# Performance work log

Measured on AMD Instinct MI355X. Metric: run time of the kernel, lower is better.

## Reference

```python
import jax, jax.numpy as jnp
import numpy as np

B, S, D, H, HD = 4, 1024, 512, 8, 64  # batch, seq_len, hidden_dim, n_heads, head_dim
N_DIL = min(5, H)


def _head_masks(seq_len: int, n_heads: int) -> jnp.ndarray:
    """Log-sparse banded+dilated masks, shape [n_heads, S, S] (bool)."""
    i = jnp.arange(seq_len)
    diff = jnp.abs(i[:, None] - i[None, :])  # [S, S]
    masks = jnp.stack([
        (diff <= 2 ** h) | (diff % (2 ** (h + 1)) == 0)
        for h in range(N_DIL)
    ])  # [N_DIL, S, S]
    idx = [min(h, N_DIL - 1) for h in range(n_heads)]
    return masks[jnp.asarray(idx)]  # [H, S, S]


def setup_inputs() -> dict:
    key = jax.random.key(0)
    ks = jax.random.split(key, 9)
    sc = 0.02
    return {
        "x": jax.random.normal(ks[0], (B, S, D), jnp.float32),
        "Wq": jax.random.normal(ks[1], (H, D, HD), jnp.float32) * sc,
        "bq": jax.random.normal(ks[2], (H, HD), jnp.float32) * sc,
        "Wk": jax.random.normal(ks[3], (H, D, HD), jnp.float32) * sc,
        "bk": jax.random.normal(ks[4], (H, HD), jnp.float32) * sc,
        "Wv": jax.random.normal(ks[5], (H, D, HD), jnp.float32) * sc,
        "bv": jax.random.normal(ks[6], (H, HD), jnp.float32) * sc,
        "Wo": jax.random.normal(ks[7], (D, D), jnp.float32) * sc,
        "bo": jax.random.normal(ks[8], (D,), jnp.float32) * sc,
    }


def reference(x, Wq, bq, Wk, bk, Wv, bv, Wo, bo):
    b, s, d = x.shape
    h, _, hd = Wq.shape
    # Per-head projections (batched over heads).
    q = jnp.einsum("bsd,hde->bhse", x, Wq) + bq[None, :, None, :]
    k = jnp.einsum("bsd,hde->bhse", x, Wk) + bk[None, :, None, :]
    v = jnp.einsum("bsd,hde->bhse", x, Wv) + bv[None, :, None, :]
    scores = jnp.einsum("bhse,bhte->bhst", q, k) / (hd ** 0.5)
    mask = _head_masks(s, h)  # [H, S, S] bool; diagonal always allowed
    scores = jnp.where(mask[None], scores, -jnp.inf)
    probs = jax.nn.softmax(scores, axis=-1)  # dropout is identity in eval
    out = jnp.einsum("bhst,bhte->bhse", probs, v)
    concat = out.transpose(0, 2, 1, 3).reshape(b, s, d)  # heads concatenated
    return concat @ Wo + bo
```

## Files before the change

### kernel.cpp

```cpp
#include <hip/hip_runtime.h>

typedef unsigned short u16;
typedef unsigned int u32;
typedef __attribute__((ext_vector_type(8))) __bf16 bf16x8;
typedef __attribute__((ext_vector_type(4))) float f32x4;
typedef __attribute__((ext_vector_type(16))) float f32x16;
typedef __attribute__((ext_vector_type(4))) u32 u32x4;

#if __has_builtin(__builtin_amdgcn_exp2f)
#define EXP2F(x) __builtin_amdgcn_exp2f(x)
#else
#define EXP2F(x) exp2f(x)
#endif

#define SC_Q 0.18033688011112042f

static __device__ __forceinline__ u16 f2bf(float f) {
  unsigned u = __builtin_bit_cast(unsigned, f);
  u += 0x7fffu + ((u >> 16) & 1u);
  return (u16)(u >> 16);
}
static __device__ __forceinline__ float bf2f(u16 v) {
  return __builtin_bit_cast(float, (u32)v << 16);
}

static __device__ __forceinline__ f32x4 mfma16(bf16x8 a, bf16x8 b, f32x4 c) {
  return __builtin_amdgcn_mfma_f32_16x16x32_bf16(a, b, c, 0, 0, 0);
}
static __device__ __forceinline__ f32x16 mfma32(bf16x8 a, bf16x8 b, f32x16 c) {
  return __builtin_amdgcn_mfma_f32_32x32x16_bf16(a, b, c, 0, 0, 0);
}

static __device__ __forceinline__ u32 cvtpk(float lo, float hi_) {
  u32 r;
  asm("v_cvt_pk_bf16_f32 %0, %1, %2" : "=v"(r) : "v"(lo), "v"(hi_));
  return r;
}

static __device__ __forceinline__ void barrier_raw() {
  asm volatile("" ::: "memory");
  __builtin_amdgcn_s_barrier();
  asm volatile("" ::: "memory");
}

static __device__ __forceinline__ void gload_lds16(const u16* g, u16* l) {
  __builtin_amdgcn_global_load_lds((const __attribute__((address_space(1))) u32*)g,
                                   (__attribute__((address_space(3))) u32*)l, 16, 0, 0);
}

__global__ void pack_w_kernel(const float* __restrict__ Wq, const float* __restrict__ Wk,
                              const float* __restrict__ Wv, const float* __restrict__ Wo,
                              const float* __restrict__ bq, const float* __restrict__ bk,
                              const float* __restrict__ bv, u16* __restrict__ BTqkv,
                              u16* __restrict__ BTo, float* __restrict__ bqkv) {
  int idx = blockIdx.x * 256 + threadIdx.x;
  if (idx < 1536 * 512) {
    int n = idx >> 9, d = idx & 511;
    int t = n >> 9, rem = n & 511;
    int h = rem >> 6, e = rem & 63;
    const float* W = (t == 0) ? Wq : ((t == 1) ? Wk : Wv);
    float sc = (t == 0) ? SC_Q : 1.0f;
    BTqkv[idx] = f2bf(W[((size_t)h * 512 + d) * 64 + e] * sc);
  } else if (idx < 1536 * 512 + 512 * 512) {
    int j = idx - 1536 * 512;
    int n = j >> 9, d = j & 511;
    BTo[j] = f2bf(Wo[(size_t)d * 512 + n]);
  } else if (idx < 1536 * 512 + 512 * 512 + 1536) {
    int j = idx - (1536 * 512 + 512 * 512);
    int t = j >> 9, rem = j & 511;
    float v = (t == 0 ? bq : (t == 1 ? bk : bv))[rem];
    bqkv[j] = v * (t == 0 ? SC_Q : 1.0f);
  }
}

__global__ __launch_bounds__(256) void gemm_qkv_kernel(const float* __restrict__ X,
                                                       const u16* __restrict__ BT,
                                                       const float* __restrict__ bias,
                                                       u16* __restrict__ QK,
                                                       u16* __restrict__ Vtl) {
  __shared__ __align__(16) u16 Al[2][128 * 64];
  __shared__ __align__(16) u16 Bl[2][64 * 64];
  const int K = 512;
  const int tid = threadIdx.x;
  const int w = tid >> 6, lane = tid & 63, g = lane >> 4, i = lane & 15;
  const int m0 = blockIdx.x * 128, n0 = blockIdx.y * 64;
  const int wr = (w >> 1) * 64, wc = (w & 1) * 32;

  f32x4 acc[4][2];
#pragma unroll
  for (int a = 0; a < 4; ++a)
#pragma unroll
    for (int b = 0; b < 2; ++b) acc[a][b] = f32x4{0.f, 0.f, 0.f, 0.f};

  const float* xg[4];
#pragma unroll
  for (int it = 0; it < 4; ++it) {
    const int slot = it * 256 + tid;
    xg[it] = X + (size_t)(m0 + (slot >> 3)) * K + (slot & 7) * 8;
  }
  const u16* bgp[2];
#pragma unroll
  for (int it = 0; it < 2; ++it) {
    const int slot = it * 256 + tid;
    bgp[it] = BT + (size_t)(n0 + (slot >> 3)) * K + (slot & 7) * 8;
  }

  float4 a0[4], a1[4];
#pragma unroll
  for (int it = 0; it < 4; ++it) {
    a0[it] = *reinterpret_cast<const float4*>(xg[it]);
    a1[it] = *reinterpret_cast<const float4*>(xg[it] + 4);
  }
#pragma unroll
  for (int it = 0; it < 2; ++it) gload_lds16(bgp[it], &Bl[0][(it * 256 + tid) * 8]);
  asm volatile("s_waitcnt vmcnt(2)" ::: "memory");
#pragma unroll
  for (int it = 0; it < 4; ++it) {
    u32x4 pk = {cvtpk(a0[it].x, a0[it].y), cvtpk(a0[it].z, a0[it].w),
                cvtpk(a1[it].x, a1[it].y), cvtpk(a1[it].z, a1[it].w)};
    *reinterpret_cast<u32x4*>(&Al[0][(it * 256 + tid) * 8]) = pk;
  }
  asm volatile("s_waitcnt lgkmcnt(0)" ::: "memory");

  int cur = 0;
  for (int t = 0; t < 8; ++t) {
    const int k0 = t * 64;
    if (t < 7) {
#pragma unroll
      for (int it = 0; it < 4; ++it) {
        a0[it] = *reinterpret_cast<const float4*>(xg[it] + k0 + 64);
        a1[it] = *reinterpret_cast<const float4*>(xg[it] + k0 + 68);
      }
#pragma unroll
      for (int it = 0; it < 2; ++it)
        gload_lds16(bgp[it] + k0 + 64, &Bl[cur ^ 1][(it * 256 + tid) * 8]);
      asm volatile("s_waitcnt vmcnt(10)" ::: "memory");
    } else {
      asm volatile("s_waitcnt vmcnt(0)" ::: "memory");
    }
    barrier_raw();
#pragma unroll
    for (int ks = 0; ks < 2; ++ks) {
      bf16x8 af[4], bf[2];
#pragma unroll
      for (int mf = 0; mf < 4; ++mf)
        af[mf] = *reinterpret_cast<const bf16x8*>(
            &Al[cur][(wr + mf * 16 + i) * 64 + ks * 32 + 8 * g]);
#pragma unroll
      for (int nf = 0; nf < 2; ++nf)
        bf[nf] = *reinterpret_cast<const bf16x8*>(
            &Bl[cur][(wc + nf * 16 + i) * 64 + ks * 32 + 8 * g]);
#pragma unroll
      for (int mf = 0; mf < 4; ++mf)
#pragma unroll
        for (int nf = 0; nf < 2; ++nf) acc[mf][nf] = mfma16(af[mf], bf[nf], acc[mf][nf]);
    }
    if (t < 7) {
      asm volatile("s_waitcnt vmcnt(2)" ::: "memory");
#pragma unroll
      for (int it = 0; it < 4; ++it) {
        u32x4 pk = {cvtpk(a0[it].x, a0[it].y), cvtpk(a0[it].z, a0[it].w),
                    cvtpk(a1[it].x, a1[it].y), cvtpk(a1[it].z, a1[it].w)};
        *reinterpret_cast<u32x4*>(&Al[cur ^ 1][(it * 256 + tid) * 8]) = pk;
      }
      asm volatile("s_waitcnt lgkmcnt(0)" ::: "memory");
    }
    barrier_raw();
    cur ^= 1;
  }

  if (n0 < 1024) {
#pragma unroll
    for (int nf = 0; nf < 2; ++nf) {
      const int col = n0 + wc + nf * 16 + i;
      const float bb = bias[col];
#pragma unroll
      for (int mf = 0; mf < 4; ++mf) {
#pragma unroll
        for (int r = 0; r < 4; ++r) {
          const int row = m0 + wr + mf * 16 + 4 * g + r;
          QK[(size_t)row * 1024 + col] = f2bf(acc[mf][nf][r] + bb);
        }
      }
    }
  } else {
    const int b = m0 >> 10;
    const int s0b = (m0 & 1023) + wr;
#pragma unroll
    for (int nf = 0; nf < 2; ++nf) {
      const int col = n0 + wc + nf * 16 + i;
      const float bb = bias[col];
      const int vcol = col - 1024;
      const size_t rowb = (size_t)(b * 512 + vcol) * 1024;
#pragma unroll
      for (int mf = 0; mf < 4; ++mf) {
        u16 pk[4];
#pragma unroll
        for (int r = 0; r < 4; ++r) pk[r] = f2bf(acc[mf][nf][r] + bb);
        const int ss = s0b + mf * 16 + 4 * g;
        *reinterpret_cast<uint2*>(&Vtl[rowb + ss]) = *reinterpret_cast<const uint2*>(pk);
      }
    }
  }
}

__global__ __launch_bounds__(256) void attn3_kernel(const u16* __restrict__ QK,
                                                    const u16* __restrict__ Vt,
                                                    u16* __restrict__ Opart16,
                                                    float* __restrict__ mlpart) {
  __shared__ __align__(16) u16 Kl[2][4096];
  __shared__ __align__(16) u16 Vl[2][4096];

  const int tid = threadIdx.x;
  const int w = tid >> 6, lane = tid & 63;
  const int col = lane & 31, hi = lane >> 5;
  const int h = blockIdx.x;
  const int zz = blockIdx.z;
  const int b = zz >> 1, s = zz & 1;
  const int bh = b * 8 + h;
  const int q0w = blockIdx.y * 128 + w * 32;
  const int kvlo = s * 512;
  const int hm = (h < 4) ? h : 4;
  const int band = 1 << hm;
  const int modm = (2 << hm) - 1;
  const int qrow = q0w + col;

  bf16x8 qf[4];
  const size_t qoff = (size_t)(b * 1024 + qrow) * 1024 + h * 64 + 8 * hi;
#pragma unroll
  for (int et = 0; et < 4; ++et)
    qf[et] = *reinterpret_cast<const bf16x8*>(QK + qoff + 16 * et);

  float bias[16];
#pragma unroll
  for (int r = 0; r < 16; ++r) {
    int c = (r & 3) + 8 * (r >> 2) + 4 * hi;
    bias[r] = (((qrow - c) & modm) == 0) ? 0.f : -1e30f;
  }

  f32x16 accO0 = {}, accO1 = {};
  float m_run = -1e30f, l_run = 0.f;

  const int slot0 = tid, slot1 = tid + 256;
  const int kj0 = slot0 >> 3, keb0 = (slot0 & 7) ^ (kj0 & 7);
  const int kj1 = slot1 >> 3, keb1 = (slot1 & 7) ^ (kj1 & 7);
  const u16* kg0 = QK + (size_t)(b * 1024 + kj0) * 1024 + 512 + h * 64 + keb0 * 8;
  const u16* kg1 = QK + (size_t)(b * 1024 + kj1) * 1024 + 512 + h * 64 + keb1 * 8;
  const u16* vg0 = Vt + (size_t)(bh * 64 + kj0) * 1024 + keb0 * 8;
  const u16* vg1 = Vt + (size_t)(bh * 64 + kj1) * 1024 + keb1 * 8;

#define STAGE3(bi, kv0)                                                 \
  do {                                                                  \
    gload_lds16(kg0 + (size_t)(kv0) * 1024, &Kl[bi][slot0 * 8]);        \
    gload_lds16(kg1 + (size_t)(kv0) * 1024, &Kl[bi][slot1 * 8]);        \
    gload_lds16(vg0 + (kv0), &Vl[bi][slot0 * 8]);                       \
    gload_lds16(vg1 + (kv0), &Vl[bi][slot1 * 8]);                       \
  } while (0)

  STAGE3(0, kvlo);
  int buf = 0;

  for (int t = 0; t < 8; ++t) {
    const int kv0 = kvlo + t * 64;
    if (t < 7) {
      STAGE3(buf ^ 1, kv0 + 64);
      asm volatile("s_waitcnt vmcnt(4)" ::: "memory");
    } else {
      asm volatile("s_waitcnt vmcnt(0)" ::: "memory");
    }
    barrier_raw();

    const u16* Kb = Kl[buf];
    const u16* Vb = Vl[buf];

    f32x16 s0 = {}, s1 = {};
    __builtin_amdgcn_s_setprio(1);
#pragma unroll
    for (int et = 0; et < 4; ++et) {
      const int sw = ((2 * et + hi) ^ (col & 7)) << 3;
      bf16x8 kf0 = *reinterpret_cast<const bf16x8*>(&Kb[col * 64 + sw]);
      bf16x8 kf1 = *reinterpret_cast<const bf16x8*>(&Kb[(col + 32) * 64 + sw]);
      s0 = mfma32(kf0, qf[et], s0);
      s1 = mfma32(kf1, qf[et], s1);
    }
    __builtin_amdgcn_s_setprio(0);

    float p[32];
    const int dq = qrow - kv0;
    const bool near = (q0w <= kv0 + 63 + band) && (kv0 <= q0w + 31 + band);
    if (near) {
#pragma unroll
      for (int r = 0; r < 16; ++r) {
        const int c = (r & 3) + 8 * (r >> 2) + 4 * hi;
        int d0 = dq - c, d1 = d0 - 32;
        d0 = d0 < 0 ? -d0 : d0;
        d1 = d1 < 0 ? -d1 : d1;
        p[r] = (d0 <= band) ? s0[r] : s0[r] + bias[r];
        p[r + 16] = (d1 <= band) ? s1[r] : s1[r] + bias[r];
      }
    } else {
#pragma unroll
      for (int r = 0; r < 16; ++r) {
        p[r] = s0[r] + bias[r];
        p[r + 16] = s1[r] + bias[r];
      }
    }

    float tr[16];
#pragma unroll
    for (int j = 0; j < 16; ++j) tr[j] = fmaxf(p[j], p[j + 16]);
#pragma unroll
    for (int st = 8; st >= 1; st >>= 1)
#pragma unroll
      for (int j = 0; j < st; ++j) tr[j] = fmaxf(tr[j], tr[j + st]);
    float mu = fmaxf(tr[0], __shfl_xor(tr[0], 32));

    if (__any(mu > m_run + 8.f)) {
      float mn = fmaxf(m_run, mu);
      float corr = EXP2F(m_run - mn);
      m_run = mn;
      l_run *= corr;
#pragma unroll
      for (int j = 0; j < 16; ++j) {
        accO0[j] *= corr;
        accO1[j] *= corr;
      }
    }

#pragma unroll
    for (int j = 0; j < 32; ++j) p[j] = EXP2F(p[j] - m_run);
    float ts[16];
#pragma unroll
    for (int j = 0; j < 16; ++j) ts[j] = p[j] + p[j + 16];
#pragma unroll
    for (int st = 8; st >= 1; st >>= 1)
#pragma unroll
      for (int j = 0; j < st; ++j) ts[j] += ts[j + st];
    l_run += ts[0] + __shfl_xor(ts[0], 32);

#pragma unroll
    for (int kt = 0; kt < 4; ++kt) {
      const float* pp = (kt < 2) ? p : p + 16;
      const int R = (kt & 1) * 8;
      u32 A0 = cvtpk(pp[R + 0], pp[R + 1]);
      u32 A1 = cvtpk(pp[R + 2], pp[R + 3]);
      u32 B0 = cvtpk(pp[R + 4], pp[R + 5]);
      u32 B1 = cvtpk(pp[R + 6], pp[R + 7]);
      u32 t0 = __shfl_xor(hi ? A0 : B0, 32);
      u32 t1 = __shfl_xor(hi ? A1 : B1, 32);
      u32 w0 = hi ? t0 : A0;
      u32 w1 = hi ? t1 : A1;
      u32 w2 = hi ? B0 : t0;
      u32 w3 = hi ? B1 : t1;
      u32x4 pu = {w0, w1, w2, w3};
      bf16x8 paf = __builtin_bit_cast(bf16x8, pu);
      const int jb = 2 * kt + hi;
      __builtin_amdgcn_s_setprio(1);
      {
        const int erow = col;
        bf16x8 vf = *reinterpret_cast<const bf16x8*>(&Vb[erow * 64 + ((jb ^ (erow & 7)) << 3)]);
        accO0 = mfma32(paf, vf, accO0);
      }
      {
        const int erow = 32 + col;
        bf16x8 vf = *reinterpret_cast<const bf16x8*>(&Vb[erow * 64 + ((jb ^ (erow & 7)) << 3)]);
        accO1 = mfma32(paf, vf, accO1);
      }
      __builtin_amdgcn_s_setprio(0);
    }

    barrier_raw();
    buf ^= 1;
  }
#undef STAGE3

  const size_t obase = (size_t)(s * 32 + bh) * 1024 + q0w;
  if (lane < 32) {
    float2 ml2 = {m_run, l_run};
    *reinterpret_cast<float2*>(&mlpart[(obase + col) * 2]) = ml2;
  }
#pragma unroll
  for (int r = 0; r < 16; ++r) {
    const int c = (r & 3) + 8 * (r >> 2) + 4 * hi;
    u16* orow = Opart16 + (obase + c) * 64;
    orow[col] = f2bf(accO0[r]);
    orow[32 + col] = f2bf(accO1[r]);
  }
}

__global__ __launch_bounds__(256) void gemm_out_kernel(const u16* __restrict__ Opart16,
                                                       const float* __restrict__ mlpart,
                                                       const u16* __restrict__ BT,
                                                       const float* __restrict__ bias,
                                                       float* __restrict__ Cf) {
  __shared__ __align__(16) u16 Al[2][64 * 64];
  __shared__ __align__(16) u16 Bl[2][64 * 64];
  const int K = 512;
  const int tid = threadIdx.x;
  const int w = tid >> 6, lane = tid & 63, g = lane >> 4, i = lane & 15;
  const int m0 = blockIdx.x * 64, n0 = blockIdx.y * 64;
  const int wr = (w >> 1) * 32, wc = (w & 1) * 32;

  f32x4 acc[2][2];
#pragma unroll
  for (int a = 0; a < 2; ++a)
#pragma unroll
    for (int b = 0; b < 2; ++b) acc[a][b] = f32x4{0.f, 0.f, 0.f, 0.f};

  size_t R0[2];
  int cb8[2];
#pragma unroll
  for (int it = 0; it < 2; ++it) {
    const int slot = it * 256 + tid;
    const int r_in = slot >> 3;
    cb8[it] = (slot & 7) * 8;
    const int grow = m0 + r_in;
    const int b2 = grow >> 10, qr = grow & 1023;
    R0[it] = (size_t)(b2 * 8) * 1024 + qr;
  }
  const u16* bgp[2];
#pragma unroll
  for (int it = 0; it < 2; ++it) {
    const int slot = it * 256 + tid;
    bgp[it] = BT + (size_t)(n0 + (slot >> 3)) * K + (slot & 7) * 8;
  }

  uint4 aO[2][2];
  float2 aml[2][2];

#define LOAD_A(t)                                                                     \
  do {                                                                                \
    _Pragma("unroll") for (int it = 0; it < 2; ++it) {                                \
      _Pragma("unroll") for (int s2 = 0; s2 < 2; ++s2) {                              \
        const size_t rb = R0[it] + (size_t)(s2 * 32 + (t)) * 1024;                    \
        aO[it][s2] = *reinterpret_cast<const uint4*>(&Opart16[rb * 64 + cb8[it]]);    \
        aml[it][s2] = *reinterpret_cast<const float2*>(&mlpart[rb * 2]);              \
      }                                                                               \
    }                                                                                 \
  } while (0)

#define COMBINE_WRITE(bi)                                                             \
  do {                                                                                \
    _Pragma("unroll") for (int it = 0; it < 2; ++it) {                                \
      const float mA = aml[it][0].x, lA = aml[it][0].y;                               \
      const float mB = aml[it][1].x, lB = aml[it][1].y;                               \
      const float M2 = fmaxf(mA, mB);                                                 \
      const float wA = EXP2F(mA - M2), wB = EXP2F(mB - M2);                           \
      const float inv = 1.0f / (lA * wA + lB * wB);                                   \
      const float sA = wA * inv, sB = wB * inv;                                       \
      const u32* oa = reinterpret_cast<const u32*>(&aO[it][0]);                       \
      const u32* ob = reinterpret_cast<const u32*>(&aO[it][1]);                       \
      float c[8];                                                                     \
      _Pragma("unroll") for (int q = 0; q < 4; ++q) {                                 \
        c[2 * q] = bf2f((u16)(oa[q] & 0xffff)) * sA + bf2f((u16)(ob[q] & 0xffff)) * sB; \
        c[2 * q + 1] = bf2f((u16)(oa[q] >> 16)) * sA + bf2f((u16)(ob[q] >> 16)) * sB; \
      }                                                                               \
      u32x4 pk = {cvtpk(c[0], c[1]), cvtpk(c[2], c[3]), cvtpk(c[4], c[5]),            \
                  cvtpk(c[6], c[7])};                                                 \
      *reinterpret_cast<u32x4*>(&Al[bi][(it * 256 + tid) * 8]) = pk;                  \
    }                                                                                 \
  } while (0)

  LOAD_A(0);
#pragma unroll
  for (int it = 0; it < 2; ++it) gload_lds16(bgp[it], &Bl[0][(it * 256 + tid) * 8]);
  asm volatile("s_waitcnt vmcnt(2)" ::: "memory");
  COMBINE_WRITE(0);
  asm volatile("s_waitcnt lgkmcnt(0)" ::: "memory");

  int cur = 0;
  for (int t = 0; t < 8; ++t) {
    if (t < 7) {
      LOAD_A(t + 1);
#pragma unroll
      for (int it = 0; it < 2; ++it)
        gload_lds16(bgp[it] + t * 64 + 64, &Bl[cur ^ 1][(it * 256 + tid) * 8]);
      asm volatile("s_waitcnt vmcnt(10)" ::: "memory");
    } else {
      asm volatile("s_waitcnt vmcnt(0)" ::: "memory");
    }
    barrier_raw();
#pragma unroll
    for (int ks = 0; ks < 2; ++ks) {
      bf16x8 af[2], bf[2];
#pragma unroll
      for (int mf = 0; mf < 2; ++mf)
        af[mf] = *reinterpret_cast<const bf16x8*>(
            &Al[cur][(wr + mf * 16 + i) * 64 + ks * 32 + 8 * g]);
#pragma unroll
      for (int nf = 0; nf < 2; ++nf)
        bf[nf] = *reinterpret_cast<const bf16x8*>(
            &Bl[cur][(wc + nf * 16 + i) * 64 + ks * 32 + 8 * g]);
#pragma unroll
      for (int mf = 0; mf < 2; ++mf)
#pragma unroll
        for (int nf = 0; nf < 2; ++nf) acc[mf][nf] = mfma16(af[mf], bf[nf], acc[mf][nf]);
    }
    if (t < 7) {
      asm volatile("s_waitcnt vmcnt(2)" ::: "memory");
      COMBINE_WRITE(cur ^ 1);
      asm volatile("s_waitcnt lgkmcnt(0)" ::: "memory");
    }
    barrier_raw();
    cur ^= 1;
  }
#undef LOAD_A
#undef COMBINE_WRITE

#pragma unroll
  for (int nf = 0; nf < 2; ++nf) {
    const int col = n0 + wc + nf * 16 + i;
    const float bb = bias[col];
#pragma unroll
    for (int mf = 0; mf < 2; ++mf) {
#pragma unroll
      for (int r = 0; r < 4; ++r) {
        const int row = m0 + wr + mf * 16 + 4 * g + r;
        Cf[(size_t)row * 512 + col] = acc[mf][nf][r] + bb;
      }
    }
  }
}

extern "C" void kernel_launch(void* const* d_in, const int* in_sizes, int n_in,
                              void* d_out, int out_size, void* d_ws, size_t ws_size,
                              hipStream_t stream) {
  const float* x = (const float*)d_in[0];
  const float* Wq = (const float*)d_in[1];
  const float* bq = (const float*)d_in[2];
  const float* Wk = (const float*)d_in[3];
  const float* bk = (const float*)d_in[4];
  const float* Wv = (const float*)d_in[5];
  const float* bv = (const float*)d_in[6];
  const float* Wo = (const float*)d_in[7];
  const float* bo = (const float*)d_in[8];
  float* out = (float*)d_out;

  char* ws = (char*)d_ws;
  u16* BTqkv = (u16*)(ws + (4u << 20));
  u16* BTo = (u16*)(ws + (6u << 20));
  float* bqkv = (float*)(ws + (7u << 20));
  u16* QK = (u16*)(ws + (8u << 20));
  u16* Vtl = (u16*)(ws + (21u << 20));
  u16* Opart16 = (u16*)(ws + (32u << 20));
  float* mlpart = (float*)(ws + (56u << 20));

  const int NW = 1536 * 512 + 512 * 512 + 1536;
  pack_w_kernel<<<(NW + 255) / 256, 256, 0, stream>>>(Wq, Wk, Wv, Wo, bq, bk, bv, BTqkv,
                                                      BTo, bqkv);

  gemm_qkv_kernel<<<dim3(32, 24), 256, 0, stream>>>(x, BTqkv, bqkv, QK, Vtl);

  attn3_kernel<<<dim3(8, 8, 8), 256, 0, stream>>>(QK, Vtl, Opart16, mlpart);

  gemm_out_kernel<<<dim3(64, 8), 256, 0, stream>>>(Opart16, mlpart, BTo, bo, out);
}
```

Before: 63.47 us.

## Split heads 4-7 attention into dilated and band kernels with permuted V layout

Heads 4-7 share the dilation-32 plus band-16 mask, so their attention is split into two specialized kernels. attnD computes the stride-32 dilated part over residue classes using a permuted V copy written by the QKV GEMM. attnB computes the band part |d| between 1 and 16 over a 64-key window. The generic attn3 kernel now covers only heads 0-3. This avoids scanning many masked-out tiles, at the cost of an extra scattered V write and two more launches, and it relies on the partial-softmax merge in gemm_out to combine the split segments.

After: 80.00 us. 1.26x slower.

```diff
diff --git a/kernel.cpp b/kernel.cpp
--- a/kernel.cpp
+++ b/kernel.cpp
@@ -77,7 +77,8 @@
                                                        const u16* __restrict__ BT,
                                                        const float* __restrict__ bias,
                                                        u16* __restrict__ QK,
-                                                       u16* __restrict__ Vtl) {
+                                                       u16* __restrict__ Vtl,
+                                                       u16* __restrict__ Vtp) {
   __shared__ __align__(16) u16 Al[2][128 * 64];
   __shared__ __align__(16) u16 Bl[2][64 * 64];
   const int K = 512;
@@ -191,6 +192,10 @@
       const int col = n0 + wc + nf * 16 + i;
       const float bb = bias[col];
       const int vcol = col - 1024;
+      const int hh = vcol >> 6;
+      const int hmm = (hh < 4) ? hh : 4;
+      const int Mlog = hmm + 1;
+      const int NcH = 1024 >> Mlog;
       const size_t rowb = (size_t)(b * 512 + vcol) * 1024;
 #pragma unroll
       for (int mf = 0; mf < 4; ++mf) {
@@ -199,6 +204,12 @@
         for (int r = 0; r < 4; ++r) pk[r] = f2bf(acc[mf][nf][r] + bb);
         const int ss = s0b + mf * 16 + 4 * g;
         *reinterpret_cast<uint2*>(&Vtl[rowb + ss]) = *reinterpret_cast<const uint2*>(pk);
+#pragma unroll
+        for (int r = 0; r < 4; ++r) {
+          const int seq = ss + r;
+          const int pidx = (seq & ((1 << Mlog) - 1)) * NcH + (seq >> Mlog);
+          Vtp[rowb + pidx] = pk[r];
+        }
       }
     }
   }
@@ -388,6 +399,263 @@
   }
 }
 
+__global__ __launch_bounds__(256) void attnD_kernel(const u16* __restrict__ QK,
+                                                    const u16* __restrict__ Vtp,
+                                                    u16* __restrict__ Opart16,
+                                                    float* __restrict__ mlpart) {
+  __shared__ __align__(16) u16 Kl[4][32 * 72];
+  __shared__ __align__(16) u16 Vl[4][64 * 40];
+
+  const int tid = threadIdx.x;
+  const int w = tid >> 6, lane = tid & 63;
+  const int col = lane & 31, hi = lane >> 5;
+  const int h = 4 + blockIdx.x;
+  const int qblk = blockIdx.y, b = blockIdx.z;
+  const int M = 32;
+  const int cls = qblk * 4 + w;
+  const int bh = b * 8 + h;
+
+  for (int sl = lane; sl < 256; sl += 64) {
+    const int kj = sl >> 3, eb = sl & 7;
+    const int physk = cls + kj * M;
+    bf16x8 kreg = *reinterpret_cast<const bf16x8*>(
+        QK + (size_t)(b * 1024 + physk) * 1024 + 512 + h * 64 + eb * 8);
+    *reinterpret_cast<bf16x8*>(&Kl[w][kj * 72 + eb * 8]) = kreg;
+  }
+  for (int sl = lane; sl < 256; sl += 64) {
+    const int e = sl >> 2, tb = sl & 3;
+    bf16x8 vreg = *reinterpret_cast<const bf16x8*>(
+        Vtp + (size_t)(b * 512 + h * 64 + e) * 1024 + cls * 32 + tb * 8);
+    *reinterpret_cast<bf16x8*>(&Vl[w][e * 40 + tb * 8]) = vreg;
+  }
+
+  const int physq = cls + col * M;
+  bf16x8 qf[4];
+  const size_t qoff = (size_t)(b * 1024 + physq) * 1024 + h * 64 + 8 * hi;
+#pragma unroll
+  for (int et = 0; et < 4; ++et)
+    qf[et] = *reinterpret_cast<const bf16x8*>(QK + qoff + 16 * et);
+
+  __syncthreads();
+
+  f32x16 s0 = {};
+  __builtin_amdgcn_s_setprio(1);
+#pragma unroll
+  for (int et = 0; et < 4; ++et) {
+    const int sw8 = (2 * et + hi) * 8;
+    bf16x8 kf0 = *reinterpret_cast<const bf16x8*>(&Kl[w][col * 72 + sw8]);
+    s0 = mfma32(kf0, qf[et], s0);
+  }
+  __builtin_amdgcn_s_setprio(0);
+
+  float p[32];
+#pragma unroll
+  for (int r = 0; r < 16; ++r) {
+    p[r] = s0[r];
+    p[r + 16] = -1e30f;
+  }
+  float tr[16];
+#pragma unroll
+  for (int j = 0; j < 16; ++j) tr[j] = fmaxf(p[j], p[j + 16]);
+#pragma unroll
+  for (int st = 8; st >= 1; st >>= 1)
+#pragma unroll
+    for (int j = 0; j < st; ++j) tr[j] = fmaxf(tr[j], tr[j + st]);
+  const float mu = fmaxf(tr[0], __shfl_xor(tr[0], 32));
+
+#pragma unroll
+  for (int j = 0; j < 32; ++j) p[j] = EXP2F(p[j] - mu);
+  float ts[16];
+#pragma unroll
+  for (int j = 0; j < 16; ++j) ts[j] = p[j] + p[j + 16];
+#pragma unroll
+  for (int st = 8; st >= 1; st >>= 1)
+#pragma unroll
+    for (int j = 0; j < st; ++j) ts[j] += ts[j + st];
+  const float l = ts[0] + __shfl_xor(ts[0], 32);
+
+  f32x16 accO0 = {}, accO1 = {};
+  const u16* Vb = &Vl[w][0];
+#pragma unroll
+  for (int kt = 0; kt < 2; ++kt) {
+    const float* pp = p;
+    const int R = (kt & 1) * 8;
+    u32 A0 = cvtpk(pp[R + 0], pp[R + 1]);
+    u32 A1 = cvtpk(pp[R + 2], pp[R + 3]);
+    u32 B0 = cvtpk(pp[R + 4], pp[R + 5]);
+    u32 B1 = cvtpk(pp[R + 6], pp[R + 7]);
+    u32 t0 = __shfl_xor(hi ? A0 : B0, 32);
+    u32 t1 = __shfl_xor(hi ? A1 : B1, 32);
+    u32 w0 = hi ? t0 : A0;
+    u32 w1 = hi ? t1 : A1;
+    u32 w2 = hi ? B0 : t0;
+    u32 w3 = hi ? B1 : t1;
+    u32x4 pu = {w0, w1, w2, w3};
+    bf16x8 paf = __builtin_bit_cast(bf16x8, pu);
+    const int jb = 2 * kt + hi;
+    __builtin_amdgcn_s_setprio(1);
+    {
+      const int erow = col;
+      bf16x8 vf = *reinterpret_cast<const bf16x8*>(&Vb[erow * 40 + (jb << 3)]);
+      accO0 = mfma32(paf, vf, accO0);
+    }
+    {
+      const int erow = 32 + col;
+      bf16x8 vf = *reinterpret_cast<const bf16x8*>(&Vb[erow * 40 + (jb << 3)]);
+      accO1 = mfma32(paf, vf, accO1);
+    }
+    __builtin_amdgcn_s_setprio(0);
+  }
+
+  const size_t pb = (size_t)(1 * 32 + bh) * 1024;
+  if (lane < 32) {
+    float2 ml2 = {mu, l};
+    *reinterpret_cast<float2*>(&mlpart[(pb + physq) * 2]) = ml2;
+  }
+#pragma unroll
+  for (int r = 0; r < 16; ++r) {
+    const int cf = (r & 3) + 8 * (r >> 2) + 4 * hi;
+    const int physr = cls + cf * M;
+    u16* orow = Opart16 + (pb + physr) * 64;
+    orow[col] = f2bf(accO0[r]);
+    orow[32 + col] = f2bf(accO1[r]);
+  }
+}
+
+__global__ __launch_bounds__(256) void attnB_kernel(const u16* __restrict__ QK,
+                                                    const u16* __restrict__ Vtl,
+                                                    u16* __restrict__ Opart16,
+                                                    float* __restrict__ mlpart) {
+  __shared__ __align__(16) u16 Kl[4][64 * 72];
+  __shared__ __align__(16) u16 Vl[4][64 * 72];
+
+  const int tid = threadIdx.x;
+  const int w = tid >> 6, lane = tid & 63;
+  const int col = lane & 31, hi = lane >> 5;
+  const int h = 4 + blockIdx.x;
+  const int qt = blockIdx.y, b = blockIdx.z;
+  const int bh = b * 8 + h;
+  const int band = 16;
+  const int q0w = qt * 128 + w * 32;
+  const int qrow = q0w + col;
+  int kw = q0w - 16;
+  kw = kw < 0 ? 0 : (kw > 960 ? 960 : kw);
+
+  for (int sl = tid; sl < 2048; sl += 256) {
+    const int wv = sl >> 9, s9 = sl & 511;
+    int kwv = qt * 128 + wv * 32 - 16;
+    kwv = kwv < 0 ? 0 : (kwv > 960 ? 960 : kwv);
+    const int kj = s9 >> 3, eb = s9 & 7;
+    bf16x8 kreg = *reinterpret_cast<const bf16x8*>(
+        QK + (size_t)(b * 1024 + kwv + kj) * 1024 + 512 + h * 64 + eb * 8);
+    *reinterpret_cast<bf16x8*>(&Kl[wv][kj * 72 + eb * 8]) = kreg;
+    bf16x8 vreg = *reinterpret_cast<const bf16x8*>(
+        Vtl + (size_t)(b * 512 + h * 64 + kj) * 1024 + kwv + eb * 8);
+    *reinterpret_cast<bf16x8*>(&Vl[wv][kj * 72 + eb * 8]) = vreg;
+  }
+
+  bf16x8 qf[4];
+  const size_t qoff = (size_t)(b * 1024 + qrow) * 1024 + h * 64 + 8 * hi;
+#pragma unroll
+  for (int et = 0; et < 4; ++et)
+    qf[et] = *reinterpret_cast<const bf16x8*>(QK + qoff + 16 * et);
+
+  f32x16 accO0 = {}, accO1 = {};
+
+  __syncthreads();
+
+  const u16* Kb = &Kl[w][0];
+  const u16* Vb = &Vl[w][0];
+
+  f32x16 s0 = {}, s1 = {};
+  __builtin_amdgcn_s_setprio(1);
+#pragma unroll
+  for (int et = 0; et < 4; ++et) {
+    const int sw8 = (2 * et + hi) * 8;
+    bf16x8 kf0 = *reinterpret_cast<const bf16x8*>(&Kb[col * 72 + sw8]);
+    bf16x8 kf1 = *reinterpret_cast<const bf16x8*>(&Kb[(col + 32) * 72 + sw8]);
+    s0 = mfma32(kf0, qf[et], s0);
+    s1 = mfma32(kf1, qf[et], s1);
+  }
+  __builtin_amdgcn_s_setprio(0);
+
+  float p[32];
+  const int dq = qrow - kw;
+#pragma unroll
+  for (int r = 0; r < 16; ++r) {
+    const int cf = (r & 3) + 8 * (r >> 2) + 4 * hi;
+    const int d0 = dq - cf, d1 = d0 - 32;
+    const int a0 = d0 < 0 ? -d0 : d0;
+    const int a1 = d1 < 0 ? -d1 : d1;
+    p[r] = (a0 >= 1 && a0 <= band) ? s0[r] : -1e30f;
+    p[r + 16] = (a1 >= 1 && a1 <= band) ? s1[r] : -1e30f;
+  }
+
+  float tr[16];
+#pragma unroll
+  for (int j = 0; j < 16; ++j) tr[j] = fmaxf(p[j], p[j + 16]);
+#pragma unroll
+  for (int st = 8; st >= 1; st >>= 1)
+#pragma unroll
+    for (int j = 0; j < st; ++j) tr[j] = fmaxf(tr[j], tr[j + st]);
+  const float mu = fmaxf(tr[0], __shfl_xor(tr[0], 32));
+
+#pragma unroll
+  for (int j = 0; j < 32; ++j) p[j] = EXP2F(p[j] - mu);
+  float ts[16];
+#pragma unroll
+  for (int j = 0; j < 16; ++j) ts[j] = p[j] + p[j + 16];
+#pragma unroll
+  for (int st = 8; st >= 1; st >>= 1)
+#pragma unroll
+    for (int j = 0; j < st; ++j) ts[j] += ts[j + st];
+  const float l = ts[0] + __shfl_xor(ts[0], 32);
+
+#pragma unroll
+  for (int kt = 0; kt < 4; ++kt) {
+    const float* pp = (kt < 2) ? p : p + 16;
+    const int R = (kt & 1) * 8;
+    u32 A0 = cvtpk(pp[R + 0], pp[R + 1]);
+    u32 A1 = cvtpk(pp[R + 2], pp[R + 3]);
+    u32 B0 = cvtpk(pp[R + 4], pp[R + 5]);
+    u32 B1 = cvtpk(pp[R + 6], pp[R + 7]);
+    u32 t0 = __shfl_xor(hi ? A0 : B0, 32);
+    u32 t1 = __shfl_xor(hi ? A1 : B1, 32);
+    u32 w0 = hi ? t0 : A0;
+    u32 w1 = hi ? t1 : A1;
+    u32 w2 = hi ? B0 : t0;
+    u32 w3 = hi ? B1 : t1;
+    u32x4 pu = {w0, w1, w2, w3};
+    bf16x8 paf = __builtin_bit_cast(bf16x8, pu);
+    const int jb = 2 * kt + hi;
+    __builtin_amdgcn_s_setprio(1);
+    {
+      const int erow = col;
+      bf16x8 vf = *reinterpret_cast<const bf16x8*>(&Vb[erow * 72 + (jb << 3)]);
+      accO0 = mfma32(paf, vf, accO0);
+    }
+    {
+      const int erow = 32 + col;
+      bf16x8 vf = *reinterpret_cast<const bf16x8*>(&Vb[erow * 72 + (jb << 3)]);
+      accO1 = mfma32(paf, vf, accO1);
+    }
+    __builtin_amdgcn_s_setprio(0);
+  }
+
+  const size_t pb = (size_t)bh * 1024;
+  if (lane < 32) {
+    float2 ml2 = {mu, l};
+    *reinterpret_cast<float2*>(&mlpart[(pb + qrow) * 2]) = ml2;
+  }
+#pragma unroll
+  for (int r = 0; r < 16; ++r) {
+    const int cf = (r & 3) + 8 * (r >> 2) + 4 * hi;
+    u16* orow = Opart16 + (pb + q0w + cf) * 64;
+    orow[col] = f2bf(accO0[r]);
+    orow[32 + col] = f2bf(accO1[r]);
+  }
+}
+
 __global__ __launch_bounds__(256) void gemm_out_kernel(const u16* __restrict__ Opart16,
                                                        const float* __restrict__ mlpart,
                                                        const u16* __restrict__ BT,
@@ -542,6 +810,7 @@
   float* bqkv = (float*)(ws + (7u << 20));
   u16* QK = (u16*)(ws + (8u << 20));
   u16* Vtl = (u16*)(ws + (21u << 20));
+  u16* Vtp = (u16*)(ws + (25u << 20));
   u16* Opart16 = (u16*)(ws + (32u << 20));
   float* mlpart = (float*)(ws + (56u << 20));
 
@@ -549,9 +818,11 @@
   pack_w_kernel<<<(NW + 255) / 256, 256, 0, stream>>>(Wq, Wk, Wv, Wo, bq, bk, bv, BTqkv,
                                                       BTo, bqkv);
 
-  gemm_qkv_kernel<<<dim3(32, 24), 256, 0, stream>>>(x, BTqkv, bqkv, QK, Vtl);
-
-  attn3_kernel<<<dim3(8, 8, 8), 256, 0, stream>>>(QK, Vtl, Opart16, mlpart);
+  gemm_qkv_kernel<<<dim3(32, 24), 256, 0, stream>>>(x, BTqkv, bqkv, QK, Vtl, Vtp);
+
+  attn3_kernel<<<dim3(4, 8, 8), 256, 0, stream>>>(QK, Vtl, Opart16, mlpart);
+  attnD_kernel<<<dim3(4, 8, 4), 256, 0, stream>>>(QK, Vtp, Opart16, mlpart);
+  attnB_kernel<<<dim3(4, 8, 4), 256, 0, stream>>>(QK, Vtl, Opart16, mlpart);
 
   gemm_out_kernel<<<dim3(64, 8), 256, 0, stream>>>(Opart16, mlpart, BTo, bo, out);
 }
```
